# Kernel optimization log

Hardware: AMD Instinct MI355X
Metric: run time of the kernel (lower is better)

Reference implementation:

```python
import jax, jax.numpy as jnp
import numpy as np

B, C, H, W = 4, 64, 128, 128
O, K = 64, 3
STRIDE, PAD = 1, 1
K2 = K * K


def conv2d(x, w, b):
    out = jax.lax.conv_general_dilated(
        x, w, (STRIDE, STRIDE), [(PAD, PAD), (PAD, PAD)],
        dimension_numbers=('NCHW', 'OIHW', 'NCHW'))
    return out + b[None, :, None, None]


def setup_inputs() -> dict:
    key = jax.random.key(0)
    ks = jax.random.split(key, 6)
    return {
        'x': jax.random.normal(ks[0], (B, C, H, W), jnp.float32),
        'offset_w': jax.random.normal(ks[1], (2 * K2, C, K, K), jnp.float32) * 0.01,
        'offset_b': jax.random.normal(ks[2], (2 * K2,), jnp.float32) * 0.01,
        'mask_w': jax.random.normal(ks[3], (K2, C, K, K), jnp.float32) * 0.01,
        'mask_b': jnp.zeros((K2,), jnp.float32),
        'deform_w': jax.random.normal(ks[4], (O, C, K, K), jnp.float32) * (1.0 / np.sqrt(C * K2)),
        'deform_b': jax.random.normal(ks[5], (O,), jnp.float32) * 0.01,
    }


def _deform_conv(x, offset, mask, w, b):
    Bn, Cn, Hin, Win = x.shape
    Ho, Wo = offset.shape[2], offset.shape[3]
    off = offset.reshape(Bn, K2, 2, Ho, Wo)
    ky = jnp.repeat(jnp.arange(K), K)   # kernel row offset per location k
    kx = jnp.tile(jnp.arange(K), K)     # kernel col offset per location k
    yo = jnp.arange(Ho) * STRIDE - PAD
    xo = jnp.arange(Wo) * STRIDE - PAD
    # sampling positions [B,K2,Ho,Wo]
    py = off[:, :, 0] + ky[None, :, None, None] + yo[None, None, :, None]
    px = off[:, :, 1] + kx[None, :, None, None] + xo[None, None, None, :]
    y0 = jnp.floor(py)
    x0 = jnp.floor(px)
    wy1 = py - y0  # fractional weights
    wx1 = px - x0
    y0i = y0.astype(jnp.int32)
    x0i = x0.astype(jnp.int32)
    x_flat = x.reshape(Bn, Cn, Hin * Win)

    def corner(yi, xi, wgt):
        valid = (yi >= 0) & (yi < Hin) & (xi >= 0) & (xi < Win)
        yc = jnp.clip(yi, 0, Hin - 1)
        xc = jnp.clip(xi, 0, Win - 1)
        idx = (yc * Win + xc).reshape(Bn, -1)
        g = jnp.take_along_axis(x_flat, idx[:, None, :], axis=2)
        g = g.reshape(Bn, Cn, K2, Ho, Wo)
        return g * (wgt * valid)[:, None]

    val = (corner(y0i, x0i, (1 - wy1) * (1 - wx1))
           + corner(y0i, x0i + 1, (1 - wy1) * wx1)
           + corner(y0i + 1, x0i, wy1 * (1 - wx1))
           + corner(y0i + 1, x0i + 1, wy1 * wx1))
    val = val * mask[:, None]  # modulate, broadcast over channels
    out = jnp.einsum('bckhw,ock->bohw', val, w.reshape(w.shape[0], Cn, K2))
    return out + b[None, :, None, None]


def reference(x, offset_w, offset_b, mask_w, mask_b, deform_w, deform_b):
    offset = conv2d(x, offset_w, offset_b)
    mask = jax.nn.sigmoid(conv2d(x, mask_w, mask_b))
    return _deform_conv(x, offset, mask, deform_w, deform_b)
```

## Files before the change

kernel.cpp:

```cpp
#include <hip/hip_runtime.h>
#include <hip/hip_bf16.h>
#include <math.h>

#define BB 4
#define CC 64
#define HH 128
#define WW 128
#define HW 16384
#define CHW (CC*HW)

typedef __bf16 bf16;
typedef __attribute__((ext_vector_type(8))) __bf16 bf16x8;
typedef __attribute__((ext_vector_type(4))) __bf16 bf16x4;
typedef __attribute__((ext_vector_type(4))) float f32x4;
typedef __attribute__((ext_vector_type(4))) unsigned short u16x4;

#define MFMA(a, b, c) __builtin_amdgcn_mfma_f32_16x16x32_bf16((a), (b), (c), 0, 0, 0)

__global__ __launch_bounds__(256) void k_pre(const float* __restrict__ x,
        bf16* __restrict__ xt,
        const float* __restrict__ dw, const float* __restrict__ ow,
        const float* __restrict__ mw,
        bf16* __restrict__ wfd_hi, bf16* __restrict__ wfd_lo,
        bf16* __restrict__ wfo_hi, bf16* __restrict__ wfo_lo) {
    __shared__ float tile[64][65];
    if (blockIdx.x < 1024) {
        int b    = blockIdx.x >> 8;
        int s0   = (blockIdx.x & 255) * 64;
        int lane = threadIdx.x & 63;
        int w    = threadIdx.x >> 6;
        const float* xb = x + (size_t)b * CHW;
        #pragma unroll
        for (int r = 0; r < 16; ++r) {
            int c = w * 16 + r;
            tile[c][lane] = xb[(size_t)c * HW + s0 + lane];
        }
        __syncthreads();
        bf16* xtb = xt + (size_t)b * CHW;
        #pragma unroll
        for (int it = 0; it < 2; ++it) {
            int task = it * 256 + threadIdx.x;
            int s = task >> 3, ch0 = (task & 7) * 8;
            bf16x8 v;
            #pragma unroll
            for (int j = 0; j < 8; ++j) v[j] = (bf16)tile[ch0 + j][s];
            *(bf16x8*)&xtb[(size_t)(s0 + s) * 64 + ch0] = v;
        }
    } else {
        int idx = (blockIdx.x - 1024) * 256 + threadIdx.x;
        if (idx < 36864) {
            int j    = idx & 7;
            int lane = (idx >> 3) & 63;
            int ks   = (idx >> 9) % 18;
            int nt   = idx / (512 * 18);
            int n    = nt * 16 + (lane & 15);
            int kglob = ks * 32 + (lane >> 4) * 8 + j;
            int kk = kglob >> 6, c = kglob & 63;
            float w = dw[(n * 64 + c) * 9 + kk];
            bf16 h = (bf16)w;
            wfd_hi[idx] = h;
            wfd_lo[idx] = (bf16)(w - (float)h);
        } else {
            int idx2 = idx - 36864;
            int j    = idx2 & 7;
            int lane = (idx2 >> 3) & 63;
            int ks   = (idx2 >> 9) % 18;
            int nt   = idx2 / (512 * 18);
            int ch   = nt * 16 + (lane & 15);
            int kglob = ks * 32 + (lane >> 4) * 8 + j;
            int kk = kglob >> 6, c = kglob & 63;
            float w = 0.0f;
            if (ch < 18)      w = ow[(ch * 64 + c) * 9 + kk];
            else if (ch < 27) w = mw[((ch - 18) * 64 + c) * 9 + kk];
            bf16 h = (bf16)w;
            wfo_hi[idx2] = h;
            wfo_lo[idx2] = (bf16)(w - (float)h);
        }
    }
}

__global__ __launch_bounds__(256) void k_B(const bf16* __restrict__ xt,
        const bf16* __restrict__ wfo_hi, const bf16* __restrict__ wfo_lo,
        const float* __restrict__ ob, const float* __restrict__ mb,
        bf16* __restrict__ sampw_g, unsigned short* __restrict__ sampo_g) {
    __shared__ float om_s[27 * 64];

    int bid = (blockIdx.x & 7) * 128 + (blockIdx.x >> 3);
    int pos0 = bid * 64;
    int wo0 = pos0 & 127;
    int ho  = (pos0 >> 7) & 127;
    int b   = pos0 >> 14;
    int t = threadIdx.x, wave = t >> 6, lane = t & 63;
    int m = lane & 15, g = lane >> 4;
    const bf16* xtb = xt + (size_t)b * CHW;

    {
        int st = wave;
        f32x4 acc0 = {0.f, 0.f, 0.f, 0.f};
        f32x4 acc1 = {0.f, 0.f, 0.f, 0.f};
        const bf16x8* bh0 = (const bf16x8*)wfo_hi + lane;
        const bf16x8* bl0 = (const bf16x8*)wfo_lo + lane;
        const bf16x8* bh1 = (const bf16x8*)wfo_hi + 18 * 64 + lane;
        const bf16x8* bl1 = (const bf16x8*)wfo_lo + 18 * 64 + lane;
        #pragma unroll
        for (int kk = 0; kk < 9; ++kk) {
            int y  = ho + kk / 3 - 1;
            int xx = wo0 + st * 16 + m + (kk % 3) - 1;
            bf16x8 ae = {};
            bf16x8 ao = {};
            if ((unsigned)y < 128u && (unsigned)xx < 128u) {
                const bf16* bp = xtb + ((size_t)(y * 128 + xx) << 6);
                ae = *(const bf16x8*)(bp + g * 8);
                ao = *(const bf16x8*)(bp + 32 + g * 8);
            }
            int ks0 = 2 * kk, ks1 = 2 * kk + 1;
            acc0 = MFMA(ae, bh0[ks0 * 64], acc0);
            acc0 = MFMA(ae, bl0[ks0 * 64], acc0);
            acc0 = MFMA(ao, bh0[ks1 * 64], acc0);
            acc0 = MFMA(ao, bl0[ks1 * 64], acc0);
            acc1 = MFMA(ae, bh1[ks0 * 64], acc1);
            acc1 = MFMA(ae, bl1[ks0 * 64], acc1);
            acc1 = MFMA(ao, bh1[ks1 * 64], acc1);
            acc1 = MFMA(ao, bl1[ks1 * 64], acc1);
        }
        int p64 = st * 16 + g * 4;
        float bias0 = ob[m];
        #pragma unroll
        for (int r = 0; r < 4; ++r)
            om_s[m * 64 + p64 + r] = acc0[r] + bias0;
        int ch1 = 16 + m;
        if (ch1 < 27) {
            float bias1 = (ch1 < 18) ? ob[ch1] : mb[ch1 - 18];
            #pragma unroll
            for (int r = 0; r < 4; ++r) {
                float v = acc1[r] + bias1;
                if (ch1 >= 18) v = 1.0f / (1.0f + __expf(-v));
                om_s[ch1 * 64 + p64 + r] = v;
            }
        }
    }
    __syncthreads();

    bf16* swg = sampw_g + (size_t)bid * 576 * 4;
    unsigned short* sog = sampo_g + (size_t)bid * 576 * 4;
    for (int task = t; task < 576; task += 256) {
        int p64 = task / 9, k = task - p64 * 9;
        float dy = om_s[(2 * k) * 64 + p64];
        float dx = om_s[(2 * k + 1) * 64 + p64];
        float mk = om_s[(18 + k) * 64 + p64];
        float py = (float)(ho - 1 + k / 3) + dy;
        float px = (float)(wo0 + p64 - 1 + (k % 3)) + dx;
        float y0f = floorf(py), x0f = floorf(px);
        float fy = py - y0f, fx = px - x0f;
        int y0 = (int)y0f, x0 = (int)x0f;
        int y1 = y0 + 1,  x1 = x0 + 1;
        bool vy0 = (unsigned)y0 < 128u, vy1 = (unsigned)y1 < 128u;
        bool vx0 = (unsigned)x0 < 128u, vx1 = (unsigned)x1 < 128u;
        int y0c = min(max(y0, 0), 127), y1c = min(max(y1, 0), 127);
        int x0c = min(max(x0, 0), 127), x1c = min(max(x1, 0), 127);
        bf16x4 wv;
        wv.x = (bf16)((vy0 && vx0) ? mk * (1.f - fy) * (1.f - fx) : 0.f);
        wv.y = (bf16)((vy0 && vx1) ? mk * (1.f - fy) * fx         : 0.f);
        wv.z = (bf16)((vy1 && vx0) ? mk * fy * (1.f - fx)         : 0.f);
        wv.w = (bf16)((vy1 && vx1) ? mk * fy * fx                 : 0.f);
        u16x4 ov;
        ov.x = (unsigned short)(y0c * 128 + x0c);
        ov.y = (unsigned short)(y0c * 128 + x1c);
        ov.z = (unsigned short)(y1c * 128 + x0c);
        ov.w = (unsigned short)(y1c * 128 + x1c);
        *(bf16x4*)&swg[task * 4] = wv;
        *(u16x4*)&sog[task * 4] = ov;
    }
}

__global__ __launch_bounds__(256) void k_D(const bf16* __restrict__ xt,
        const bf16* __restrict__ wfd_hi,
        const bf16* __restrict__ sampw_g, const unsigned short* __restrict__ sampo_g,
        const float* __restrict__ db, float* __restrict__ out) {
    __shared__ __align__(16) bf16 a_s[18 * 64 * 8];

    int bid = (blockIdx.x & 7) * 128 + (blockIdx.x >> 3);
    int pos0 = bid * 64;
    int wo0 = pos0 & 127;
    int ho  = (pos0 >> 7) & 127;
    int b   = pos0 >> 14;
    int t = threadIdx.x, wave = t >> 6, lane = t & 63;
    int m = lane & 15, g = lane >> 4;
    const bf16* xtb = xt + (size_t)b * CHW;

    const bf16x8* bhd = (const bf16x8*)wfd_hi + (size_t)wave * 18 * 64 + lane;
    int fle = ((m ^ g) + (g << 4)) * 8;
    int flo = ((m ^ g ^ 4) + (g << 4)) * 8;

    int khalf = t >> 7;
    int prow  = (t >> 3) & 15;
    int c8    = (t & 7) * 8;
    int kpar  = c8 >> 5;
    int gch   = (c8 & 31) >> 3;
    int flw   = (prow ^ gch ^ (kpar << 2)) + (gch << 4);
    char* abw = (char*)a_s + (flw << 4);
    const bf16* swb = sampw_g + (size_t)bid * 576 * 4;
    const unsigned short* sob = sampo_g + (size_t)bid * 576 * 4;

    for (int st = 0; st < 4; ++st) {
        int taskbase = (st * 16 + prow) * 9;
        auto gather1 = [&](int kk) {
            int task = taskbase + kk;
            bf16x4 wb = *(const bf16x4*)&swb[task * 4];
            u16x4  o4 = *(const u16x4*)&sob[task * 4];
            bf16x8 v00 = *(const bf16x8*)&xtb[((int)o4.x << 6) + c8];
            bf16x8 v01 = *(const bf16x8*)&xtb[((int)o4.y << 6) + c8];
            bf16x8 v10 = *(const bf16x8*)&xtb[((int)o4.z << 6) + c8];
            bf16x8 v11 = *(const bf16x8*)&xtb[((int)o4.w << 6) + c8];
            float w00 = (float)wb.x, w01 = (float)wb.y;
            float w10 = (float)wb.z, w11 = (float)wb.w;
            bf16x8 hv;
            #pragma unroll
            for (int j = 0; j < 8; ++j) {
                float r = w00 * (float)v00[j] + w01 * (float)v01[j]
                        + w10 * (float)v10[j] + w11 * (float)v11[j];
                hv[j] = (bf16)r;
            }
            int ks = 2 * kk + kpar;
            *(bf16x8*)(abw + (ks << 10)) = hv;
        };
        if (!khalf) {
            #pragma unroll
            for (int kk = 0; kk < 5; ++kk) gather1(kk);
        } else {
            #pragma unroll
            for (int kk = 5; kk < 9; ++kk) gather1(kk);
        }
        __syncthreads();

        f32x4 acc = {0.f, 0.f, 0.f, 0.f};
        __builtin_amdgcn_s_setprio(1);
        #pragma unroll
        for (int kk = 0; kk < 9; ++kk) {
            bf16x8 a0 = *(const bf16x8*)&a_s[(2 * kk) * 512 + fle];
            bf16x8 a1 = *(const bf16x8*)&a_s[(2 * kk + 1) * 512 + flo];
            acc = MFMA(a0, bhd[(2 * kk) * 64], acc);
            acc = MFMA(a1, bhd[(2 * kk + 1) * 64], acc);
        }
        __builtin_amdgcn_s_setprio(0);
        int o = wave * 16 + m;
        float bias = db[o];
        float4 vv = {acc[0] + bias, acc[1] + bias, acc[2] + bias, acc[3] + bias};
        *(float4*)&out[((size_t)(b * 64 + o)) * HW + ho * 128 + wo0 + st * 16 + g * 4] = vv;
        if (st < 3) __syncthreads();
    }
}

extern "C" void kernel_launch(void* const* d_in, const int* in_sizes, int n_in,
                              void* d_out, int out_size, void* d_ws, size_t ws_size,
                              hipStream_t stream) {
    const float* x   = (const float*)d_in[0];
    const float* ow  = (const float*)d_in[1];
    const float* ob  = (const float*)d_in[2];
    const float* mw  = (const float*)d_in[3];
    const float* mb  = (const float*)d_in[4];
    const float* dw  = (const float*)d_in[5];
    const float* db  = (const float*)d_in[6];
    float* out = (float*)d_out;

    bf16* xt = (bf16*)d_ws;
    bf16* wfd_hi = xt + (size_t)BB * HW * CC;
    bf16* wfd_lo = wfd_hi + 36864;
    bf16* wfo_hi = wfd_lo + 36864;
    bf16* wfo_lo = wfo_hi + 18432;
    bf16* sampw_g = wfo_lo + 18432;
    unsigned short* sampo_g = (unsigned short*)(sampw_g + (size_t)1024 * 576 * 4);

    k_pre<<<1024 + 216, 256, 0, stream>>>(x, xt, dw, ow, mw, wfd_hi, wfd_lo, wfo_hi, wfo_lo);
    k_B<<<1024, 256, 0, stream>>>(xt, wfo_hi, wfo_lo, ob, mb, sampw_g, sampo_g);
    k_D<<<1024, 256, 0, stream>>>(xt, wfd_hi, sampw_g, sampo_g, db, out);
}
```

Measured before the change: 124.9 us.

## Fuse offset/mask conv with deformable gather-GEMM into one kernel

```diff
diff --git a/kernel.cpp b/kernel.cpp
--- a/kernel.cpp
+++ b/kernel.cpp
@@ -27,19 +27,24 @@
     if (blockIdx.x < 1024) {
         int b    = blockIdx.x >> 8;
         int s0   = (blockIdx.x & 255) * 64;
-        int lane = threadIdx.x & 63;
-        int w    = threadIdx.x >> 6;
+        int t    = threadIdx.x;
         const float* xb = x + (size_t)b * CHW;
         #pragma unroll
-        for (int r = 0; r < 16; ++r) {
-            int c = w * 16 + r;
-            tile[c][lane] = xb[(size_t)c * HW + s0 + lane];
+        for (int it = 0; it < 4; ++it) {
+            int task = it * 256 + t;
+            int c    = task >> 4;
+            int col4 = (task & 15) * 4;
+            float4 v = *(const float4*)&xb[(size_t)c * HW + s0 + col4];
+            tile[c][col4 + 0] = v.x;
+            tile[c][col4 + 1] = v.y;
+            tile[c][col4 + 2] = v.z;
+            tile[c][col4 + 3] = v.w;
         }
         __syncthreads();
         bf16* xtb = xt + (size_t)b * CHW;
         #pragma unroll
         for (int it = 0; it < 2; ++it) {
-            int task = it * 256 + threadIdx.x;
+            int task = it * 256 + t;
             int s = task >> 3, ch0 = (task & 7) * 8;
             bf16x8 v;
             #pragma unroll
@@ -79,14 +84,18 @@
     }
 }
 
-__global__ __launch_bounds__(256) void k_B(const bf16* __restrict__ xt,
+__global__ __launch_bounds__(256) void k_fused(const bf16* __restrict__ xt,
         const bf16* __restrict__ wfo_hi, const bf16* __restrict__ wfo_lo,
+        const bf16* __restrict__ wfd_hi,
         const float* __restrict__ ob, const float* __restrict__ mb,
-        bf16* __restrict__ sampw_g, unsigned short* __restrict__ sampo_g) {
-    __shared__ float om_s[27 * 64];
-
-    int bid = (blockIdx.x & 7) * 128 + (blockIdx.x >> 3);
-    int pos0 = bid * 64;
+        const float* __restrict__ db, float* __restrict__ out) {
+    __shared__ __align__(16) bf16 a_s[18 * 64 * 8];
+    __shared__ float om_s[27 * 32];
+    __shared__ __align__(8) bf16 sampw[288 * 4];
+    __shared__ __align__(8) unsigned short sampo[288 * 4];
+
+    int bid = (blockIdx.x & 7) * 256 + (blockIdx.x >> 3);
+    int pos0 = bid * 32;
     int wo0 = pos0 & 127;
     int ho  = (pos0 >> 7) & 127;
     int b   = pos0 >> 14;
@@ -95,17 +104,14 @@
     const bf16* xtb = xt + (size_t)b * CHW;
 
     {
-        int st = wave;
-        f32x4 acc0 = {0.f, 0.f, 0.f, 0.f};
-        f32x4 acc1 = {0.f, 0.f, 0.f, 0.f};
-        const bf16x8* bh0 = (const bf16x8*)wfo_hi + lane;
-        const bf16x8* bl0 = (const bf16x8*)wfo_lo + lane;
-        const bf16x8* bh1 = (const bf16x8*)wfo_hi + 18 * 64 + lane;
-        const bf16x8* bl1 = (const bf16x8*)wfo_lo + 18 * 64 + lane;
+        int st2 = wave >> 1, ntile = wave & 1;
+        f32x4 acc = {0.f, 0.f, 0.f, 0.f};
+        const bf16x8* bh = (const bf16x8*)wfo_hi + ntile * 18 * 64 + lane;
+        const bf16x8* bl = (const bf16x8*)wfo_lo + ntile * 18 * 64 + lane;
         #pragma unroll
         for (int kk = 0; kk < 9; ++kk) {
             int y  = ho + kk / 3 - 1;
-            int xx = wo0 + st * 16 + m + (kk % 3) - 1;
+            int xx = wo0 + st2 * 16 + m + (kk % 3) - 1;
             bf16x8 ae = {};
             bf16x8 ao = {};
             if ((unsigned)y < 128u && (unsigned)xx < 128u) {
@@ -114,42 +120,32 @@
                 ao = *(const bf16x8*)(bp + 32 + g * 8);
             }
             int ks0 = 2 * kk, ks1 = 2 * kk + 1;
-            acc0 = MFMA(ae, bh0[ks0 * 64], acc0);
-            acc0 = MFMA(ae, bl0[ks0 * 64], acc0);
-            acc0 = MFMA(ao, bh0[ks1 * 64], acc0);
-            acc0 = MFMA(ao, bl0[ks1 * 64], acc0);
-            acc1 = MFMA(ae, bh1[ks0 * 64], acc1);
-            acc1 = MFMA(ae, bl1[ks0 * 64], acc1);
-            acc1 = MFMA(ao, bh1[ks1 * 64], acc1);
-            acc1 = MFMA(ao, bl1[ks1 * 64], acc1);
-        }
-        int p64 = st * 16 + g * 4;
-        float bias0 = ob[m];
-        #pragma unroll
-        for (int r = 0; r < 4; ++r)
-            om_s[m * 64 + p64 + r] = acc0[r] + bias0;
-        int ch1 = 16 + m;
-        if (ch1 < 27) {
-            float bias1 = (ch1 < 18) ? ob[ch1] : mb[ch1 - 18];
+            acc = MFMA(ae, bh[ks0 * 64], acc);
+            acc = MFMA(ae, bl[ks0 * 64], acc);
+            acc = MFMA(ao, bh[ks1 * 64], acc);
+            acc = MFMA(ao, bl[ks1 * 64], acc);
+        }
+        int ch = ntile * 16 + m;
+        int p32 = st2 * 16 + g * 4;
+        if (ch < 27) {
+            float bias = (ch < 18) ? ob[ch] : mb[ch - 18];
             #pragma unroll
             for (int r = 0; r < 4; ++r) {
-                float v = acc1[r] + bias1;
-                if (ch1 >= 18) v = 1.0f / (1.0f + __expf(-v));
-                om_s[ch1 * 64 + p64 + r] = v;
+                float v = acc[r] + bias;
+                if (ch >= 18) v = 1.0f / (1.0f + __expf(-v));
+                om_s[ch * 32 + p32 + r] = v;
             }
         }
     }
     __syncthreads();
 
-    bf16* swg = sampw_g + (size_t)bid * 576 * 4;
-    unsigned short* sog = sampo_g + (size_t)bid * 576 * 4;
-    for (int task = t; task < 576; task += 256) {
-        int p64 = task / 9, k = task - p64 * 9;
-        float dy = om_s[(2 * k) * 64 + p64];
-        float dx = om_s[(2 * k + 1) * 64 + p64];
-        float mk = om_s[(18 + k) * 64 + p64];
+    for (int task = t; task < 288; task += 256) {
+        int p32 = task / 9, k = task - p32 * 9;
+        float dy = om_s[(2 * k) * 32 + p32];
+        float dx = om_s[(2 * k + 1) * 32 + p32];
+        float mk = om_s[(18 + k) * 32 + p32];
         float py = (float)(ho - 1 + k / 3) + dy;
-        float px = (float)(wo0 + p64 - 1 + (k % 3)) + dx;
+        float px = (float)(wo0 + p32 - 1 + (k % 3)) + dx;
         float y0f = floorf(py), x0f = floorf(px);
         float fy = py - y0f, fx = px - x0f;
         int y0 = (int)y0f, x0 = (int)x0f;
@@ -168,30 +164,14 @@
         ov.y = (unsigned short)(y0c * 128 + x1c);
         ov.z = (unsigned short)(y1c * 128 + x0c);
         ov.w = (unsigned short)(y1c * 128 + x1c);
-        *(bf16x4*)&swg[task * 4] = wv;
-        *(u16x4*)&sog[task * 4] = ov;
-    }
-}
-
-__global__ __launch_bounds__(256) void k_D(const bf16* __restrict__ xt,
-        const bf16* __restrict__ wfd_hi,
-        const bf16* __restrict__ sampw_g, const unsigned short* __restrict__ sampo_g,
-        const float* __restrict__ db, float* __restrict__ out) {
-    __shared__ __align__(16) bf16 a_s[18 * 64 * 8];
-
-    int bid = (blockIdx.x & 7) * 128 + (blockIdx.x >> 3);
-    int pos0 = bid * 64;
-    int wo0 = pos0 & 127;
-    int ho  = (pos0 >> 7) & 127;
-    int b   = pos0 >> 14;
-    int t = threadIdx.x, wave = t >> 6, lane = t & 63;
-    int m = lane & 15, g = lane >> 4;
-    const bf16* xtb = xt + (size_t)b * CHW;
+        *(bf16x4*)&sampw[task * 4] = wv;
+        *(u16x4*)&sampo[task * 4] = ov;
+    }
+    __syncthreads();
 
     const bf16x8* bhd = (const bf16x8*)wfd_hi + (size_t)wave * 18 * 64 + lane;
     int fle = ((m ^ g) + (g << 4)) * 8;
     int flo = ((m ^ g ^ 4) + (g << 4)) * 8;
-
     int khalf = t >> 7;
     int prow  = (t >> 3) & 15;
     int c8    = (t & 7) * 8;
@@ -199,15 +179,14 @@
     int gch   = (c8 & 31) >> 3;
     int flw   = (prow ^ gch ^ (kpar << 2)) + (gch << 4);
     char* abw = (char*)a_s + (flw << 4);
-    const bf16* swb = sampw_g + (size_t)bid * 576 * 4;
-    const unsigned short* sob = sampo_g + (size_t)bid * 576 * 4;
-
-    for (int st = 0; st < 4; ++st) {
+
+    #pragma unroll
+    for (int st = 0; st < 2; ++st) {
         int taskbase = (st * 16 + prow) * 9;
         auto gather1 = [&](int kk) {
             int task = taskbase + kk;
-            bf16x4 wb = *(const bf16x4*)&swb[task * 4];
-            u16x4  o4 = *(const u16x4*)&sob[task * 4];
+            bf16x4 wb = *(const bf16x4*)&sampw[task * 4];
+            u16x4  o4 = *(const u16x4*)&sampo[task * 4];
             bf16x8 v00 = *(const bf16x8*)&xtb[((int)o4.x << 6) + c8];
             bf16x8 v01 = *(const bf16x8*)&xtb[((int)o4.y << 6) + c8];
             bf16x8 v10 = *(const bf16x8*)&xtb[((int)o4.z << 6) + c8];
@@ -247,7 +226,7 @@
         float bias = db[o];
         float4 vv = {acc[0] + bias, acc[1] + bias, acc[2] + bias, acc[3] + bias};
         *(float4*)&out[((size_t)(b * 64 + o)) * HW + ho * 128 + wo0 + st * 16 + g * 4] = vv;
-        if (st < 3) __syncthreads();
+        if (st < 1) __syncthreads();
     }
 }
 
@@ -268,10 +247,7 @@
     bf16* wfd_lo = wfd_hi + 36864;
     bf16* wfo_hi = wfd_lo + 36864;
     bf16* wfo_lo = wfo_hi + 18432;
-    bf16* sampw_g = wfo_lo + 18432;
-    unsigned short* sampo_g = (unsigned short*)(sampw_g + (size_t)1024 * 576 * 4);
 
     k_pre<<<1024 + 216, 256, 0, stream>>>(x, xt, dw, ow, mw, wfd_hi, wfd_lo, wfo_hi, wfo_lo);
-    k_B<<<1024, 256, 0, stream>>>(xt, wfo_hi, wfo_lo, ob, mb, sampw_g, sampo_g);
-    k_D<<<1024, 256, 0, stream>>>(xt, wfd_hi, sampw_g, sampo_g, db, out);
+    k_fused<<<(BB * HW) / 32, 256, 0, stream>>>(xt, wfo_hi, wfo_lo, wfd_hi, ob, mb, db, out);
 }
```

Result: slower. 127.7 us (+2.3%).
